# Performance work log

Hardware: AMD Instinct MI355X
Metric: run time of the kernel (lower is better)

## Reference

```python
import jax, jax.numpy as jnp
import numpy as np


def _conv3x3(x, w):
    # x: [N,C,H,W], w: [O,I,3,3], stride 1, padding 1 -> SAME
    return jax.lax.conv_general_dilated(
        x, w, window_strides=(1, 1), padding='SAME',
        dimension_numbers=('NCHW', 'OIHW', 'NCHW'))


def setup_inputs() -> dict:
    key = jax.random.key(0)
    k1, k2, k3, k4 = jax.random.split(key, 4)
    # He-like init scale for 3x3 convs
    x = jax.random.normal(k1, (8, 1, 512, 512), dtype=jnp.float32)
    w1 = jax.random.normal(k2, (8, 1, 3, 3), dtype=jnp.float32) * (2.0 / (1 * 9)) ** 0.5
    wmid = jax.random.normal(k3, (18, 8, 8, 3, 3), dtype=jnp.float32) * (2.0 / (8 * 9)) ** 0.5
    w20 = jax.random.normal(k4, (1, 8, 3, 3), dtype=jnp.float32) * (2.0 / (8 * 9)) ** 0.5
    return {'x': x, 'w1': w1, 'wmid': wmid, 'w20': w20}


def reference(x, w1, wmid, w20):
    y = jax.nn.relu(_conv3x3(x, w1))  # conv1 + relu
    # conv2..conv19: 18 identical 8->8 conv+relu layers, scanned over stacked weights
    def body(y, w):
        return jax.nn.relu(_conv3x3(y, w)), None
    y, _ = jax.lax.scan(body, y, wmid)
    return _conv3x3(y, w20)  # conv20, no relu
```

## Files before the change

### kernel.cpp

```cpp
#include <hip/hip_runtime.h>

typedef _Float16 f16;
typedef _Float16 f16x8 __attribute__((ext_vector_type(8)));
typedef _Float16 f16x4 __attribute__((ext_vector_type(4)));
typedef float v4f __attribute__((ext_vector_type(4)));

constexpr int H = 512, W = 512, NB = 8;
constexpr int ROWS = 514;
constexpr int COLS = 528;
constexpr int CH = 8;
constexpr size_t ROWBYTES = (size_t)COLS * CH * 2;
constexpr size_t PLANE_ELEMS = (size_t)ROWS * COLS * CH;
constexpr size_t PLANE_BYTES = PLANE_ELEMS * 2;

constexpr int RSP = 145;
constexpr int RSPC = RSP * CH;
constexpr int LDS_ROWB = RSP * 16;
constexpr int WTAB_L = 3072;

constexpr int FRSP = 81;
constexpr int FRSPC = FRSP * CH;
constexpr int FROWB = FRSP * 16;
constexpr int INR = 12;
constexpr int ARR = 10;

__device__ __forceinline__ void gload_lds16(const void* g, void* l) {
    __builtin_amdgcn_global_load_lds(
        (const __attribute__((address_space(1))) unsigned int*)g,
        (__attribute__((address_space(3))) unsigned int*)l, 16, 0, 0);
}
__device__ __forceinline__ void gload_lds4(const void* g, void* l) {
    __builtin_amdgcn_global_load_lds(
        (const __attribute__((address_space(1))) unsigned int*)g,
        (__attribute__((address_space(3))) unsigned int*)l, 4, 0, 0);
}

__global__ void zero_borders(f16* __restrict__ base, size_t set_stride) {
    const int i = blockIdx.x * 256 + threadIdx.x;
    if (i >= 9248) return;
    const int img = blockIdx.y, set = blockIdx.z;
    int row, col;
    if (i < 1056) { row = (i < 528) ? 0 : 513; col = (i < 528) ? i : i - 528; }
    else {
        const int j = i - 1056;
        row = 1 + (j >> 4);
        const int c4 = j & 15;
        col = (c4 < 8) ? c4 : 512 + c4;
    }
    f16x8 z = {};
    f16* p = base + (size_t)set * set_stride + ((size_t)img * ROWS + row) * COLS * CH + (size_t)col * CH;
    *(f16x8*)p = z;
}

__global__ void build_wtab(const float* __restrict__ wmid,
                           const float* __restrict__ w20,
                           f16* __restrict__ wtab) {
    const int l = blockIdx.x;
    const int lane = threadIdx.x;
    const float* wt = (l < 18) ? wmid + (size_t)l * 576 : w20;
    const int COUT = (l < 18) ? 8 : 1;
    const int n = lane & 15, q = lane >> 4;
#pragma unroll
    for (int g = 0; g < 3; ++g) {
        const int t = g * 4 + q;
        f16x8 hv, lv;
#pragma unroll
        for (int j = 0; j < 8; ++j) {
            float wv = 0.f;
            if (n < 8) {
                if (t <= 8 && n < COUT) wv = wt[(n * 8 + j) * 9 + t];
            } else {
                const int o = n - 8;
                if (t >= 3 && o < COUT) wv = wt[(o * 8 + j) * 9 + (t - 3)];
            }
            const f16 h = (f16)wv;
            hv[j] = h;
            lv[j] = (f16)(wv - (float)h);
        }
        f16* dst = wtab + (size_t)l * WTAB_L + (g * 2) * 512 + lane * 8;
        *(f16x8*)dst = hv;
        *(f16x8*)(dst + 512) = lv;
    }
}

__global__ __launch_bounds__(256) void conv1_kernel(
    const float* __restrict__ in, const float* __restrict__ wt,
    f16* __restrict__ out)
{
    const int x0 = (blockIdx.x * 64 + threadIdx.x) * 4;
    const int y  = blockIdx.y * 4 + threadIdx.y;
    const int b  = blockIdx.z;
    const float* inb = in + (size_t)b * H * W;

    float patch[3][6];
#pragma unroll
    for (int r = 0; r < 3; ++r) {
        const int iy = y - 1 + r;
        if (iy >= 0 && iy < H) {
            const float* rp = inb + (size_t)iy * W;
            const float4 v = *(const float4*)(rp + x0);
            patch[r][1] = v.x; patch[r][2] = v.y; patch[r][3] = v.z; patch[r][4] = v.w;
            patch[r][0] = (x0 > 0)     ? rp[x0 - 1] : 0.f;
            patch[r][5] = (x0 + 4 < W) ? rp[x0 + 4] : 0.f;
        } else {
#pragma unroll
            for (int k = 0; k < 6; ++k) patch[r][k] = 0.f;
        }
    }

    float acc[8][4];
#pragma unroll
    for (int o = 0; o < 8; ++o) {
        const float* wo = wt + o * 9;
        float a0 = 0.f, a1 = 0.f, a2 = 0.f, a3 = 0.f;
#pragma unroll
        for (int r = 0; r < 3; ++r)
#pragma unroll
            for (int k = 0; k < 3; ++k) {
                const float wv = wo[r * 3 + k];
                a0 = fmaf(wv, patch[r][k + 0], a0);
                a1 = fmaf(wv, patch[r][k + 1], a1);
                a2 = fmaf(wv, patch[r][k + 2], a2);
                a3 = fmaf(wv, patch[r][k + 3], a3);
            }
        acc[o][0] = a0; acc[o][1] = a1; acc[o][2] = a2; acc[o][3] = a3;
    }

#pragma unroll
    for (int j = 0; j < 4; ++j) {
        f16x8 hv;
#pragma unroll
        for (int o = 0; o < 8; ++o)
            hv[o] = (f16)fmaxf(acc[o][j], 0.f);
        const size_t off = (((size_t)b * ROWS + (y + 1)) * COLS + (x0 + j + 8)) * CH;
        *(f16x8*)(out + off) = hv;
    }
}

__global__ __launch_bounds__(256, 4) void conv2fused(
    const f16* __restrict__ in,
    const f16* __restrict__ wtA, const f16* __restrict__ wtB,
    f16* __restrict__ outp)
{
    __shared__ __align__(16) f16 aring[ARR * FRSPC];
    __shared__ __align__(16) f16 inring[INR * FRSPC];

    const int wave = threadIdx.x >> 6, lane = threadIdx.x & 63;
    const int img = blockIdx.x, xt = blockIdx.y;
    const int x0 = xt * 64;
    const int base = blockIdx.z * 32;

    f16x8 ahiW[3], aloW[3], bhiW[3], bloW[3];
#pragma unroll
    for (int g = 0; g < 3; ++g) {
        const f16* wa = wtA + (g * 2) * 512 + lane * 8;
        ahiW[g] = *(const f16x8*)wa;  aloW[g] = *(const f16x8*)(wa + 512);
        const f16* wb = wtB + (g * 2) * 512 + lane * 8;
        bhiW[g] = *(const f16x8*)wb;  bloW[g] = *(const f16x8*)(wb + 512);
    }

    const char* src = (const char*)in + (size_t)img * PLANE_BYTES + (size_t)x0 * 16;

    auto stage = [&](int r0, int cnt) {
        for (int rr = wave; rr < cnt; rr += 4) {
            const int row = r0 + rr;
            const int rowc = min(max(row, 0), 513);
            const int slot = ((row % INR) + INR) % INR;
            const char* gs = src + (size_t)rowc * ROWBYTES;
            char* ld = (char*)inring + slot * FROWB;
            gload_lds16(gs + lane * 16, ld);
            if (lane < 16) gload_lds16(gs + 1024 + lane * 16, ld + 1024);
        }
    };

    const int n = lane & 15, q = lane >> 4;
    int tyv[3], txv[3];
#pragma unroll
    for (int g = 0; g < 3; ++g) { const int t = g * 4 + q; tyv[g] = t / 3 - 1; txv[g] = t % 3 - 1; }
    const int rowoff = q >> 1, choff = (q & 1) * 4;
    const bool xe0 = (xt == 0), xe7 = (xt == 7);

    auto computeA = [&](int rA) {
        __builtin_amdgcn_s_setprio(1);
        int irow[3];
#pragma unroll
        for (int g = 0; g < 3; ++g) {
            const int r = rA + tyv[g];
            irow[g] = (((r % INR) + INR) % INR) * FRSPC;
        }
        const int gyA = rA + rowoff;
        const int wrow = (gyA % ARR) * FRSPC;
        const bool zr = (gyA == 0) || (gyA == 513);
#pragma unroll
        for (int s = 0; s < 5; ++s) {
            v4f acc = {0.f,0.f,0.f,0.f}, acc2 = {0.f,0.f,0.f,0.f};
#pragma unroll
            for (int g = 0; g < 3; ++g) {
                const f16x8 xv = *(const f16x8*)&inring[irow[g] + (16 * s + n + txv[g]) * CH];
                acc  = __builtin_amdgcn_mfma_f32_16x16x32_f16(ahiW[g], xv, acc,  0, 0, 0);
                acc2 = __builtin_amdgcn_mfma_f32_16x16x32_f16(aloW[g], xv, acc2, 0, 0, 0);
            }
            const v4f res = acc + acc2;
            f16x4 hv;
#pragma unroll
            for (int c = 0; c < 4; ++c) hv[c] = (f16)fmaxf(res[c], 0.f);
            if (zr || (xe0 && s == 0 && n == 7) || (xe7 && s == 4 && n == 8)) {
                hv[0] = (f16)0.f; hv[1] = (f16)0.f; hv[2] = (f16)0.f; hv[3] = (f16)0.f;
            }
            *(f16x4*)&aring[wrow + (16 * s + n) * CH + choff] = hv;
        }
        __builtin_amdgcn_s_setprio(0);
    };

    auto computeB = [&](int rB) {
        __builtin_amdgcn_s_setprio(1);
        int brow[3];
#pragma unroll
        for (int g = 0; g < 3; ++g) brow[g] = ((rB + tyv[g]) % ARR) * FRSPC;
        const int gyB = rB + rowoff;
        f16* orow = outp + ((size_t)img * ROWS + gyB) * COLS * CH + (size_t)(x0 + 8) * CH + choff;
#pragma unroll
        for (int s = 0; s < 4; ++s) {
            v4f acc = {0.f,0.f,0.f,0.f}, acc2 = {0.f,0.f,0.f,0.f};
#pragma unroll
            for (int g = 0; g < 3; ++g) {
                const f16x8 xv = *(const f16x8*)&aring[brow[g] + (16 * s + n + txv[g] + 8) * CH];
                acc  = __builtin_amdgcn_mfma_f32_16x16x32_f16(bhiW[g], xv, acc,  0, 0, 0);
                acc2 = __builtin_amdgcn_mfma_f32_16x16x32_f16(bloW[g], xv, acc2, 0, 0, 0);
            }
            const v4f res = acc + acc2;
            f16x4 hv;
#pragma unroll
            for (int c = 0; c < 4; ++c) hv[c] = (f16)fmaxf(res[c], 0.f);
            *(f16x4*)(orow + (size_t)(16 * s + n) * CH) = hv;
        }
        __builtin_amdgcn_s_setprio(0);
    };

    stage(base - 1, 12);
    __syncthreads();
    if (wave == 0) computeA(base);

    for (int t = 0; t < 4; ++t) {
        computeA(base + 8 * t + 2 + 2 * wave);
        __syncthreads();
        if (t < 3) stage(base + 8 * t + 11, 8);
        computeB(base + 8 * t + 1 + 2 * wave);
        __syncthreads();
    }
}

template<bool RELU, bool FINAL>
__global__ __launch_bounds__(256) void convmfma(
    const f16* __restrict__ in, const f16* __restrict__ wtab_l,
    f16* __restrict__ outp, float* __restrict__ out_final)
{
    __shared__ __align__(16) f16 lds[2][10 * RSPC];

    const int wave = threadIdx.x >> 6, lane = threadIdx.x & 63;
    const int img = blockIdx.x;
    const int x0 = blockIdx.y * 128;
    const int ybase = blockIdx.z * 32;

    f16x8 bhi[3], blo[3];
#pragma unroll
    for (int g = 0; g < 3; ++g) {
        const f16* wp = wtab_l + (g * 2) * 512 + lane * 8;
        bhi[g] = *(const f16x8*)wp;
        blo[g] = *(const f16x8*)(wp + 512);
    }

    const char* src = (const char*)in + (size_t)img * PLANE_BYTES + (size_t)x0 * 16;
    auto stage = [&](int buf, int y0) {
        char* dst = (char*)&lds[buf][0];
        for (int qq = wave; qq < 30; qq += 4) {
            const int r = qq / 3, c = qq % 3;
            const char* gs = src + (size_t)(y0 + r) * ROWBYTES;
            char* ld = dst + r * LDS_ROWB;
            if (c < 2) gload_lds16(gs + c * 1024 + lane * 16, ld + c * 1024);
            else       gload_lds4(gs + 2048 + lane * 4, ld + 2048);
        }
    };

    const int n = lane & 15, q = lane >> 4, m = lane & 15;
    int abase[3];
#pragma unroll
    for (int g = 0; g < 3; ++g) {
        const int t = g * 4 + q;
        const int ty = t / 3 - 1, tx = t % 3 - 1;
        abase[g] = (2 * wave + ty + 1) * RSP + (m + tx + 8);
    }
    const int rowoff = q >> 1;
    const int choff = (q & 1) * 4;

    stage(0, ybase);
    __syncthreads();

    for (int t = 0; t < 4; ++t) {
        if (t < 3) stage((t + 1) & 1, ybase + 8 * (t + 1));
        const f16* L = &lds[t & 1][0];
        const int Y = ybase + 8 * t + 2 * wave;
#pragma unroll
        for (int s = 0; s < 8; ++s) {
            v4f acc = {0.f,0.f,0.f,0.f}, acc2 = {0.f,0.f,0.f,0.f};
#pragma unroll
            for (int g = 0; g < 3; ++g) {
                const f16x8 xv = *(const f16x8*)&L[(abase[g] + 16 * s) * CH];
                acc  = __builtin_amdgcn_mfma_f32_16x16x32_f16(bhi[g], xv, acc,  0, 0, 0);
                acc2 = __builtin_amdgcn_mfma_f32_16x16x32_f16(blo[g], xv, acc2, 0, 0, 0);
            }
            const v4f res = acc + acc2;
            if constexpr (!FINAL) {
                f16x4 hv;
#pragma unroll
                for (int c = 0; c < 4; ++c) {
                    float v = res[c];
                    if (RELU) v = fmaxf(v, 0.f);
                    hv[c] = (f16)v;
                }
                const int gy = Y + rowoff + 1;
                const int gx = x0 + 16 * s + n + 8;
                *(f16x4*)(outp + ((size_t)img * ROWS + gy) * COLS * CH + (size_t)gx * CH + choff) = hv;
            } else {
                if ((q & 1) == 0) {
                    const int gy = Y + rowoff, gx = x0 + 16 * s + n;
                    out_final[((size_t)img * H + gy) * W + gx] = res[0];
                }
            }
        }
        if (t < 3) __syncthreads();
    }
}

extern "C" void kernel_launch(void* const* d_in, const int* in_sizes, int n_in,
                              void* d_out, int out_size, void* d_ws, size_t ws_size,
                              hipStream_t stream) {
    const float* x    = (const float*)d_in[0];
    const float* w1   = (const float*)d_in[1];
    const float* wmid = (const float*)d_in[2];
    const float* w20  = (const float*)d_in[3];
    float* out = (float*)d_out;

    const size_t wtab_bytes = (size_t)19 * WTAB_L * 2;
    int g = NB;
    while (g > 1 && 2 * (size_t)g * PLANE_BYTES + wtab_bytes > ws_size) g >>= 1;

    f16* act0 = (f16*)d_ws;
    f16* act1 = act0 + (size_t)g * PLANE_ELEMS;
    f16* wtab = act1 + (size_t)g * PLANE_ELEMS;

    zero_borders<<<dim3(37, g, 2), 256, 0, stream>>>(act0, (size_t)g * PLANE_ELEMS);
    build_wtab<<<19, 64, 0, stream>>>(wmid, w20, wtab);

    for (int b0 = 0; b0 < NB; b0 += g) {
        conv1_kernel<<<dim3(2, 128, g), dim3(64, 4), 0, stream>>>(
            x + (size_t)b0 * H * W, w1, act0);
        for (int k = 0; k < 9; ++k) {
            const f16* s0 = (k & 1) ? act1 : act0;
            f16*       d0 = (k & 1) ? act0 : act1;
            conv2fused<<<dim3(g, 8, 16), 256, 0, stream>>>(
                s0, wtab + (size_t)(2 * k) * WTAB_L, wtab + (size_t)(2 * k + 1) * WTAB_L, d0);
        }
        convmfma<false, true><<<dim3(g, 4, 16), 256, 0, stream>>>(
            act1, wtab + (size_t)18 * WTAB_L, nullptr, out + (size_t)b0 * H * W);
    }
}
```

Measured before the change: 264.2 us.

## Fuse conv1 and final conv into paired fused-layer kernel variants

Re-pairs the 20 layers so conv1+conv2 and conv19+conv20 each run in the two-layer fused kernel. MODE 1 reads the fp32 input straight into the LDS ring as a split hi/lo f16 pair, and MODE 2 writes fp32 final output. This drops the standalone conv1 kernel and the separate final MFMA conv. It removes two full activation-plane round trips through global memory and one launch, at the cost of scalar fp32 staging loads in the first layer.

```diff
diff --git a/kernel.cpp b/kernel.cpp
--- a/kernel.cpp
+++ b/kernel.cpp
@@ -13,9 +13,6 @@
 constexpr size_t PLANE_ELEMS = (size_t)ROWS * COLS * CH;
 constexpr size_t PLANE_BYTES = PLANE_ELEMS * 2;
 
-constexpr int RSP = 145;
-constexpr int RSPC = RSP * CH;
-constexpr int LDS_ROWB = RSP * 16;
 constexpr int WTAB_L = 3072;
 
 constexpr int FRSP = 81;
@@ -28,11 +25,6 @@
     __builtin_amdgcn_global_load_lds(
         (const __attribute__((address_space(1))) unsigned int*)g,
         (__attribute__((address_space(3))) unsigned int*)l, 16, 0, 0);
-}
-__device__ __forceinline__ void gload_lds4(const void* g, void* l) {
-    __builtin_amdgcn_global_load_lds(
-        (const __attribute__((address_space(1))) unsigned int*)g,
-        (__attribute__((address_space(3))) unsigned int*)l, 4, 0, 0);
 }
 
 __global__ void zero_borders(f16* __restrict__ base, size_t set_stride) {
@@ -52,13 +44,15 @@
     *(f16x8*)p = z;
 }
 
-__global__ void build_wtab(const float* __restrict__ wmid,
+__global__ void build_wtab(const float* __restrict__ w1,
+                           const float* __restrict__ wmid,
                            const float* __restrict__ w20,
                            f16* __restrict__ wtab) {
     const int l = blockIdx.x;
     const int lane = threadIdx.x;
-    const float* wt = (l < 18) ? wmid + (size_t)l * 576 : w20;
-    const int COUT = (l < 18) ? 8 : 1;
+    const float* wt = (l < 18) ? wmid + (size_t)l * 576 : (l == 18 ? w20 : w1);
+    const int COUT = (l == 18) ? 1 : 8;
+    const bool c1 = (l == 19);
     const int n = lane & 15, q = lane >> 4;
 #pragma unroll
     for (int g = 0; g < 3; ++g) {
@@ -67,7 +61,10 @@
 #pragma unroll
         for (int j = 0; j < 8; ++j) {
             float wv = 0.f;
-            if (n < 8) {
+            if (c1) {
+                if (n < 8) { if (t <= 8 && j < 2) wv = wt[n * 9 + t]; }
+                else       { const int o = n - 8; if (t >= 3 && j < 2) wv = wt[o * 9 + (t - 3)]; }
+            } else if (n < 8) {
                 if (t <= 8 && n < COUT) wv = wt[(n * 8 + j) * 9 + t];
             } else {
                 const int o = n - 8;
@@ -83,64 +80,11 @@
     }
 }
 
-__global__ __launch_bounds__(256) void conv1_kernel(
-    const float* __restrict__ in, const float* __restrict__ wt,
-    f16* __restrict__ out)
-{
-    const int x0 = (blockIdx.x * 64 + threadIdx.x) * 4;
-    const int y  = blockIdx.y * 4 + threadIdx.y;
-    const int b  = blockIdx.z;
-    const float* inb = in + (size_t)b * H * W;
-
-    float patch[3][6];
-#pragma unroll
-    for (int r = 0; r < 3; ++r) {
-        const int iy = y - 1 + r;
-        if (iy >= 0 && iy < H) {
-            const float* rp = inb + (size_t)iy * W;
-            const float4 v = *(const float4*)(rp + x0);
-            patch[r][1] = v.x; patch[r][2] = v.y; patch[r][3] = v.z; patch[r][4] = v.w;
-            patch[r][0] = (x0 > 0)     ? rp[x0 - 1] : 0.f;
-            patch[r][5] = (x0 + 4 < W) ? rp[x0 + 4] : 0.f;
-        } else {
-#pragma unroll
-            for (int k = 0; k < 6; ++k) patch[r][k] = 0.f;
-        }
-    }
-
-    float acc[8][4];
-#pragma unroll
-    for (int o = 0; o < 8; ++o) {
-        const float* wo = wt + o * 9;
-        float a0 = 0.f, a1 = 0.f, a2 = 0.f, a3 = 0.f;
-#pragma unroll
-        for (int r = 0; r < 3; ++r)
-#pragma unroll
-            for (int k = 0; k < 3; ++k) {
-                const float wv = wo[r * 3 + k];
-                a0 = fmaf(wv, patch[r][k + 0], a0);
-                a1 = fmaf(wv, patch[r][k + 1], a1);
-                a2 = fmaf(wv, patch[r][k + 2], a2);
-                a3 = fmaf(wv, patch[r][k + 3], a3);
-            }
-        acc[o][0] = a0; acc[o][1] = a1; acc[o][2] = a2; acc[o][3] = a3;
-    }
-
-#pragma unroll
-    for (int j = 0; j < 4; ++j) {
-        f16x8 hv;
-#pragma unroll
-        for (int o = 0; o < 8; ++o)
-            hv[o] = (f16)fmaxf(acc[o][j], 0.f);
-        const size_t off = (((size_t)b * ROWS + (y + 1)) * COLS + (x0 + j + 8)) * CH;
-        *(f16x8*)(out + off) = hv;
-    }
-}
-
+template<int MODE>
 __global__ __launch_bounds__(256, 4) void conv2fused(
     const f16* __restrict__ in,
     const f16* __restrict__ wtA, const f16* __restrict__ wtB,
-    f16* __restrict__ outp)
+    f16* __restrict__ outp, float* __restrict__ outf)
 {
     __shared__ __align__(16) f16 aring[ARR * FRSPC];
     __shared__ __align__(16) f16 inring[INR * FRSPC];
@@ -164,12 +108,31 @@
     auto stage = [&](int r0, int cnt) {
         for (int rr = wave; rr < cnt; rr += 4) {
             const int row = r0 + rr;
-            const int rowc = min(max(row, 0), 513);
             const int slot = ((row % INR) + INR) % INR;
-            const char* gs = src + (size_t)rowc * ROWBYTES;
-            char* ld = (char*)inring + slot * FROWB;
-            gload_lds16(gs + lane * 16, ld);
-            if (lane < 16) gload_lds16(gs + 1024 + lane * 16, ld + 1024);
+            if constexpr (MODE == 1) {
+                const float* xin = (const float*)in;
+                const int iy = row - 1;
+                const bool vr = (iy >= 0) && (iy < H);
+                const float* xr = xin + (size_t)img * H * W + (size_t)(vr ? iy : 0) * W;
+                f16* ld = inring + slot * FRSPC;
+#pragma unroll
+                for (int k = 0; k < 2; ++k) {
+                    if (k == 1 && lane >= 16) continue;
+                    const int ci = 64 * k + lane;
+                    const int px = x0 - 8 + ci;
+                    const float v = (vr && px >= 0 && px < W) ? xr[px] : 0.f;
+                    const f16 h = (f16)v;
+                    f16x8 o = {};
+                    o[0] = h; o[1] = (f16)(v - (float)h);
+                    *(f16x8*)&ld[(size_t)ci * CH] = o;
+                }
+            } else {
+                const int rowc = min(max(row, 0), 513);
+                const char* gs = src + (size_t)rowc * ROWBYTES;
+                char* ld = (char*)inring + slot * FROWB;
+                gload_lds16(gs + lane * 16, ld);
+                if (lane < 16) gload_lds16(gs + 1024 + lane * 16, ld + 1024);
+            }
         }
     };
 
@@ -229,10 +192,15 @@
                 acc2 = __builtin_amdgcn_mfma_f32_16x16x32_f16(bloW[g], xv, acc2, 0, 0, 0);
             }
             const v4f res = acc + acc2;
-            f16x4 hv;
-#pragma unroll
-            for (int c = 0; c < 4; ++c) hv[c] = (f16)fmaxf(res[c], 0.f);
-            *(f16x4*)(orow + (size_t)(16 * s + n) * CH) = hv;
+            if constexpr (MODE == 2) {
+                if (choff == 0)
+                    outf[((size_t)img * H + (gyB - 1)) * W + (x0 + 16 * s + n)] = res[0];
+            } else {
+                f16x4 hv;
+#pragma unroll
+                for (int c = 0; c < 4; ++c) hv[c] = (f16)fmaxf(res[c], 0.f);
+                *(f16x4*)(orow + (size_t)(16 * s + n) * CH) = hv;
+            }
         }
         __builtin_amdgcn_s_setprio(0);
     };
@@ -247,88 +215,6 @@
         if (t < 3) stage(base + 8 * t + 11, 8);
         computeB(base + 8 * t + 1 + 2 * wave);
         __syncthreads();
-    }
-}
-
-template<bool RELU, bool FINAL>
-__global__ __launch_bounds__(256) void convmfma(
-    const f16* __restrict__ in, const f16* __restrict__ wtab_l,
-    f16* __restrict__ outp, float* __restrict__ out_final)
-{
-    __shared__ __align__(16) f16 lds[2][10 * RSPC];
-
-    const int wave = threadIdx.x >> 6, lane = threadIdx.x & 63;
-    const int img = blockIdx.x;
-    const int x0 = blockIdx.y * 128;
-    const int ybase = blockIdx.z * 32;
-
-    f16x8 bhi[3], blo[3];
-#pragma unroll
-    for (int g = 0; g < 3; ++g) {
-        const f16* wp = wtab_l + (g * 2) * 512 + lane * 8;
-        bhi[g] = *(const f16x8*)wp;
-        blo[g] = *(const f16x8*)(wp + 512);
-    }
-
-    const char* src = (const char*)in + (size_t)img * PLANE_BYTES + (size_t)x0 * 16;
-    auto stage = [&](int buf, int y0) {
-        char* dst = (char*)&lds[buf][0];
-        for (int qq = wave; qq < 30; qq += 4) {
-            const int r = qq / 3, c = qq % 3;
-            const char* gs = src + (size_t)(y0 + r) * ROWBYTES;
-            char* ld = dst + r * LDS_ROWB;
-            if (c < 2) gload_lds16(gs + c * 1024 + lane * 16, ld + c * 1024);
-            else       gload_lds4(gs + 2048 + lane * 4, ld + 2048);
-        }
-    };
-
-    const int n = lane & 15, q = lane >> 4, m = lane & 15;
-    int abase[3];
-#pragma unroll
-    for (int g = 0; g < 3; ++g) {
-        const int t = g * 4 + q;
-        const int ty = t / 3 - 1, tx = t % 3 - 1;
-        abase[g] = (2 * wave + ty + 1) * RSP + (m + tx + 8);
-    }
-    const int rowoff = q >> 1;
-    const int choff = (q & 1) * 4;
-
-    stage(0, ybase);
-    __syncthreads();
-
-    for (int t = 0; t < 4; ++t) {
-        if (t < 3) stage((t + 1) & 1, ybase + 8 * (t + 1));
-        const f16* L = &lds[t & 1][0];
-        const int Y = ybase + 8 * t + 2 * wave;
-#pragma unroll
-        for (int s = 0; s < 8; ++s) {
-            v4f acc = {0.f,0.f,0.f,0.f}, acc2 = {0.f,0.f,0.f,0.f};
-#pragma unroll
-            for (int g = 0; g < 3; ++g) {
-                const f16x8 xv = *(const f16x8*)&L[(abase[g] + 16 * s) * CH];
-                acc  = __builtin_amdgcn_mfma_f32_16x16x32_f16(bhi[g], xv, acc,  0, 0, 0);
-                acc2 = __builtin_amdgcn_mfma_f32_16x16x32_f16(blo[g], xv, acc2, 0, 0, 0);
-            }
-            const v4f res = acc + acc2;
-            if constexpr (!FINAL) {
-                f16x4 hv;
-#pragma unroll
-                for (int c = 0; c < 4; ++c) {
-                    float v = res[c];
-                    if (RELU) v = fmaxf(v, 0.f);
-                    hv[c] = (f16)v;
-                }
-                const int gy = Y + rowoff + 1;
-                const int gx = x0 + 16 * s + n + 8;
-                *(f16x4*)(outp + ((size_t)img * ROWS + gy) * COLS * CH + (size_t)gx * CH + choff) = hv;
-            } else {
-                if ((q & 1) == 0) {
-                    const int gy = Y + rowoff, gx = x0 + 16 * s + n;
-                    out_final[((size_t)img * H + gy) * W + gx] = res[0];
-                }
-            }
-        }
-        if (t < 3) __syncthreads();
     }
 }
 
@@ -341,7 +227,7 @@
     const float* w20  = (const float*)d_in[3];
     float* out = (float*)d_out;
 
-    const size_t wtab_bytes = (size_t)19 * WTAB_L * 2;
+    const size_t wtab_bytes = (size_t)20 * WTAB_L * 2;
     int g = NB;
     while (g > 1 && 2 * (size_t)g * PLANE_BYTES + wtab_bytes > ws_size) g >>= 1;
 
@@ -350,18 +236,22 @@
     f16* wtab = act1 + (size_t)g * PLANE_ELEMS;
 
     zero_borders<<<dim3(37, g, 2), 256, 0, stream>>>(act0, (size_t)g * PLANE_ELEMS);
-    build_wtab<<<19, 64, 0, stream>>>(wmid, w20, wtab);
+    build_wtab<<<20, 64, 0, stream>>>(w1, wmid, w20, wtab);
 
     for (int b0 = 0; b0 < NB; b0 += g) {
-        conv1_kernel<<<dim3(2, 128, g), dim3(64, 4), 0, stream>>>(
-            x + (size_t)b0 * H * W, w1, act0);
-        for (int k = 0; k < 9; ++k) {
-            const f16* s0 = (k & 1) ? act1 : act0;
-            f16*       d0 = (k & 1) ? act0 : act1;
-            conv2fused<<<dim3(g, 8, 16), 256, 0, stream>>>(
-                s0, wtab + (size_t)(2 * k) * WTAB_L, wtab + (size_t)(2 * k + 1) * WTAB_L, d0);
-        }
-        convmfma<false, true><<<dim3(g, 4, 16), 256, 0, stream>>>(
-            act1, wtab + (size_t)18 * WTAB_L, nullptr, out + (size_t)b0 * H * W);
-    }
-}
+        conv2fused<1><<<dim3(g, 8, 16), 256, 0, stream>>>(
+            (const f16*)(x + (size_t)b0 * H * W),
+            wtab + (size_t)19 * WTAB_L, wtab + (size_t)0 * WTAB_L,
+            act0, nullptr);
+        for (int k = 1; k <= 8; ++k) {
+            const f16* s0 = (k & 1) ? act0 : act1;
+            f16*       d0 = (k & 1) ? act1 : act0;
+            conv2fused<0><<<dim3(g, 8, 16), 256, 0, stream>>>(
+                s0, wtab + (size_t)(2 * k - 1) * WTAB_L, wtab + (size_t)(2 * k) * WTAB_L,
+                d0, nullptr);
+        }
+        conv2fused<2><<<dim3(g, 8, 16), 256, 0, stream>>>(
+            act0, wtab + (size_t)17 * WTAB_L, wtab + (size_t)18 * WTAB_L,
+            nullptr, out + (size_t)b0 * H * W);
+    }
+}
```

Measured after the change: 260.4 us. Within noise of the previous version (-1.5%).
